# Optimization experiments

Measured on AMD Instinct MI355X. Metric: run time of the kernel, lower is better.

Reference implementation:

```python
import jax, jax.numpy as jnp
import numpy as np

B, N, DIM = 8, 2048, 512
HEADS, DIM_HEAD = 8, 64
INNER = HEADS * DIM_HEAD  # 512
SCALE = DIM_HEAD ** -0.5
NEG = -1e9


def setup_inputs() -> dict:
    key = jax.random.key(0)
    ks = jax.random.split(key, 7)
    x = jax.random.normal(ks[0], (B, N, DIM), dtype=jnp.float32)
    adj = jax.random.uniform(ks[1], (B, N, N), dtype=jnp.float32)
    att_mask = jax.random.randint(ks[2], (B, 1, N, N), 0, 2).astype(jnp.bool_)
    W_gcn = jax.random.normal(ks[3], (DIM, DIM), dtype=jnp.float32) * (DIM ** -0.5)
    W_qkv = jax.random.normal(ks[4], (DIM, 3 * INNER), dtype=jnp.float32) * (DIM ** -0.5)
    W_out = jax.random.normal(ks[5], (INNER + DIM, DIM), dtype=jnp.float32) * ((INNER + DIM) ** -0.5)
    b_out = jax.random.normal(ks[6], (DIM,), dtype=jnp.float32) * 0.01
    return {"x": x, "adj": adj, "att_mask": att_mask,
            "W_gcn": W_gcn, "W_qkv": W_qkv, "W_out": W_out, "b_out": b_out}


def reference(x, adj, att_mask, W_gcn, W_qkv, W_out, b_out):
    # GCN branch: adj @ (x W_gcn)  -> [b, n, dim]
    gcn = jnp.einsum('bnj,bjd->bnd', adj, x @ W_gcn)

    # Attention branch
    qkv = x @ W_qkv                                  # [b, n, 3*inner]
    q, k, v = jnp.split(qkv, 3, axis=-1)
    split_heads = lambda t: t.reshape(B, N, HEADS, DIM_HEAD).transpose(0, 2, 1, 3)
    q, k, v = split_heads(q), split_heads(k), split_heads(v)  # [b, h, n, d]

    dots = jnp.einsum('bhid,bhjd->bhij', q, k) * SCALE        # [b, h, n, n]
    dots = jnp.where(att_mask, NEG, dots)
    attn = jax.nn.softmax(dots, axis=-1)
    att_out = jnp.einsum('bhij,bhjd->bhid', attn, v)          # [b, h, n, d]
    att_out = att_out.transpose(0, 2, 1, 3).reshape(B, N, INNER)

    out = jnp.concatenate([att_out, gcn], axis=-1)            # [b, n, inner+dim]
    return out @ W_out + b_out                                # [b, n, dim]
```

## Files before the change

kernel.cpp:

```cpp
#include <hip/hip_runtime.h>
#include <stdint.h>

#define DEVFN __device__ __forceinline__

typedef __attribute__((ext_vector_type(8))) short short8;
typedef __attribute__((ext_vector_type(4))) short short4v;
typedef __attribute__((ext_vector_type(4))) float floatx4;
typedef __attribute__((ext_vector_type(16))) float floatx16;
typedef __attribute__((ext_vector_type(4))) float vfloat4;
typedef __attribute__((ext_vector_type(2))) unsigned int uint2v;
typedef __attribute__((ext_vector_type(4))) unsigned int uint4v;

#define MFMA_BF16(a,b,c) __builtin_amdgcn_mfma_f32_16x16x32_bf16((a),(b),(c),0,0,0)
#define MFMA32_BF16(a,b,c) __builtin_amdgcn_mfma_f32_32x32x16_bf16((a),(b),(c),0,0,0)
#define GL2LDS(g,l) __builtin_amdgcn_global_load_lds((const __attribute__((address_space(1))) void*)(g), (__attribute__((address_space(3))) void*)(l), 16, 0, 0)

DEVFN unsigned short f2bf(float f){
  unsigned u = __float_as_uint(f);
  u = (u + 0x7fffu + ((u >> 16) & 1u)) >> 16;
  return (unsigned short)u;
}

DEVFN unsigned cvtpk_bf16(float lo, float hi){
  unsigned r;
  asm("v_cvt_pk_bf16_f32 %0, %1, %2" : "=v"(r) : "v"(lo), "v"(hi));
  return r;
}

__global__ void detect_kernel(const unsigned char* m, unsigned int* flag){
  if (threadIdx.x == 0) *flag = 0u;
  __syncthreads();
  int any = 0;
  for (int i = threadIdx.x; i < 4096; i += 256)
    if ((i & 3) != 0 && m[i]) any = 1;
  if (any) atomicOr(flag, 1u);
}

__global__ void prep_kernel(const float* __restrict__ x, const float* __restrict__ wg,
                            const float* __restrict__ wq, const float* __restrict__ wo,
                            const void* __restrict__ mask, const unsigned* __restrict__ flag,
                            const float* __restrict__ adj,
                            unsigned short* __restrict__ xbf, unsigned short* __restrict__ wcat,
                            unsigned short* __restrict__ woutT, unsigned* __restrict__ mp,
                            unsigned short* __restrict__ adjb)
{
  int bid = blockIdx.x, tid = threadIdx.x;
  if (bid < 8192) {
    int i = (bid*256 + tid)*4;
    vfloat4 v = *(const vfloat4*)&x[i];
    short4v c; c[0]=(short)f2bf(v[0]); c[1]=(short)f2bf(v[1]); c[2]=(short)f2bf(v[2]); c[3]=(short)f2bf(v[3]);
    *(short4v*)&xbf[i] = c;
  } else if (bid < 8192 + 4096) {
    int i = (bid - 8192)*256 + tid;
    int k = i & 511, c = i >> 9;
    float v = (c < 512) ? wg[k*512 + c] : wq[k*1536 + (c - 512)];
    if (c >= 512 && c < 1024) v *= 0.18033688f;
    wcat[c*512 + k] = (unsigned short)f2bf(v);
  } else if (bid < 8192 + 4096 + 2048) {
    int i = (bid - 12288)*256 + tid;
    int k = i & 1023, n2 = i >> 10;
    woutT[n2*1024 + k] = (unsigned short)f2bf(wo[k*512 + n2]);
  } else if (bid < 145408) {
    int j = bid - 14336;
    int e = j*256 + tid;
    int v;
    if (*flag) v = ((const unsigned char*)mask)[e];
    else       v = ((const int*)mask)[e];
    unsigned long long ball = __ballot(v != 0);
    int base = e & ~63;
    int lane = tid & 63;
    if (lane == 0)  mp[(base >> 5) + 0] = (unsigned)(ball & 0xffffffffull);
    if (lane == 32) mp[(base >> 5) + 1] = (unsigned)(ball >> 32);
  } else {
    int i = ((bid - 145408)*256 + tid)*4;
    vfloat4 v = *(const vfloat4*)&adj[i];
    short4v c; c[0]=(short)f2bf(v[0]); c[1]=(short)f2bf(v[1]); c[2]=(short)f2bf(v[2]); c[3]=(short)f2bf(v[3]);
    *(short4v*)&adjb[i] = c;
  }
}

DEVFN void gemm_kloop_bf16(const unsigned short* Ag, int lda,
                           const unsigned short* Bg, int ldb, int K,
                           short* As, short* Bs, int w, int l,
                           floatx4 (&acc)[4][4])
{
  const int wr = (w >> 1)*64, wc = (w & 1)*64;
  for (int k0 = 0; k0 < K; k0 += 32) {
    __syncthreads();
#pragma unroll
    for (int i = 0; i < 2; i++) {
      int id = (w*2 + i)*64 + l;
      int row = id >> 2, part = id & 3;
      GL2LDS(Ag + row*lda + k0 + part*8, As + (w*2 + i)*512);
      GL2LDS(Bg + row*ldb + k0 + part*8, Bs + (w*2 + i)*512);
    }
    __syncthreads();
    short8 af[4], bfr[4];
#pragma unroll
    for (int t = 0; t < 4; t++) {
      af[t]  = *(const short8*)&As[(wr + t*16 + (l & 15))*32 + ((l >> 4) << 3)];
      bfr[t] = *(const short8*)&Bs[(wc + t*16 + (l & 15))*32 + ((l >> 4) << 3)];
    }
#pragma unroll
    for (int a2 = 0; a2 < 4; a2++)
#pragma unroll
      for (int b2 = 0; b2 < 4; b2++)
        acc[a2][b2] = MFMA_BF16(af[a2], bfr[b2], acc[a2][b2]);
  }
}

__global__ __launch_bounds__(256, 2)
void gemm_ab_kernel(const unsigned short* __restrict__ xbf, const unsigned short* __restrict__ wcat,
                    unsigned short* __restrict__ xgT, unsigned short* __restrict__ Qo,
                    unsigned short* __restrict__ Ko, unsigned short* __restrict__ VTo)
{
  __shared__ short lds[16384];
  int tid = threadIdx.x, w = tid >> 6, l = tid & 63;
  int bid = blockIdx.x;
  int xcd = bid & 7, slot = bid >> 3;
  int p  = xcd + ((slot >> 4) << 3);
  int nt = slot & 15;
  int rows0 = p*128, cols0 = nt*128;

  floatx4 acc[4][4];
  const floatx4 zf = {0.f, 0.f, 0.f, 0.f};
#pragma unroll
  for (int a2 = 0; a2 < 4; a2++)
#pragma unroll
    for (int b2 = 0; b2 < 4; b2++) acc[a2][b2] = zf;

  gemm_kloop_bf16(xbf + rows0*512, 512, wcat + cols0*512, 512, 512,
                  lds, lds + 4096, w, l, acc);
  __syncthreads();

  int wr = (w >> 1)*64, wc = (w & 1)*64;
  int b = p >> 4;
  int n0 = (p & 15)*128 + wr;
  int gc0 = cols0 + wc;

  if (nt < 4 || nt >= 12) {
    short* T = lds + w*4096;
#pragma unroll
    for (int mi = 0; mi < 4; mi++)
#pragma unroll
      for (int bi = 0; bi < 4; bi++)
#pragma unroll
        for (int r = 0; r < 4; r++) {
          int rl = mi*16 + ((l >> 4) << 2) + r;
          int cl = bi*16 + (l & 15);
          T[cl*64 + ((((rl >> 3) ^ (cl & 7))) << 3) + (rl & 7)] = (short)f2bf(acc[mi][bi][r]);
        }
#pragma unroll
    for (int i = 0; i < 8; i++) {
      int chunk = i*64 + l;
      int c = chunk >> 3, s = chunk & 7;
      short8 v = *(const short8*)&T[c*64 + ((s ^ (c & 7)) << 3)];
      int rowstart = n0 + s*8;
      if (nt < 4) {
        int d = gc0 + c;
        *(short8*)&xgT[(b*512 + d)*2048 + rowstart] = v;
      } else {
        int vc = gc0 + c - 1536;
        int hh = vc >> 6, dd = vc & 63;
        *(short8*)&VTo[((b*8 + hh)*64 + dd)*2048 + rowstart] = v;
      }
    }
  } else {
    unsigned short* dst = (nt < 8) ? Qo : Ko;
    int cbase = gc0 - ((nt < 8) ? 512 : 1024);
    int hh = cbase >> 6;
#pragma unroll
    for (int mi = 0; mi < 4; mi++)
#pragma unroll
      for (int bi = 0; bi < 4; bi++)
#pragma unroll
        for (int r = 0; r < 4; r++) {
          int rowg = n0 + mi*16 + ((l >> 4) << 2) + r;
          int dd = bi*16 + (l & 15);
          dst[((b*8 + hh)*2048 + rowg)*64 + dd] = (unsigned short)f2bf(acc[mi][bi][r]);
        }
  }
}

__global__ __launch_bounds__(256, 2)
void gemm_c_f32_kernel(const float* __restrict__ adj, const unsigned short* __restrict__ xgT,
                       unsigned short* __restrict__ cat)
{
  __shared__ short lds[8192];
  int tid = threadIdx.x, w = tid >> 6, l = tid & 63;
  int bid = blockIdx.x;
  int xcd = bid & 7, slot = bid >> 3;
  int p  = xcd + ((slot >> 2) << 3);
  int nt = slot & 3;
  int b = p >> 4, mt = p & 15;
  int rows0 = mt*128, cols0 = nt*128;
  const float* Ag = adj + (size_t)b*2048*2048 + (size_t)rows0*2048;
  const unsigned short* Bg = xgT + (b*512 + cols0)*2048;

  floatx4 acc[4][4];
  const floatx4 zf = {0.f, 0.f, 0.f, 0.f};
#pragma unroll
  for (int a2 = 0; a2 < 4; a2++)
#pragma unroll
    for (int b2 = 0; b2 < 4; b2++) acc[a2][b2] = zf;

  const int wr = (w >> 1)*64, wc = (w & 1)*64;
  for (int k0 = 0; k0 < 2048; k0 += 32) {
    __syncthreads();
#pragma unroll
    for (int i = 0; i < 4; i++) {
      int id = (w*4 + i)*64 + l;
      int row = id >> 3, part = id & 7;
      vfloat4 v = *(const vfloat4*)&Ag[row*2048 + k0 + part*4];
      short4v c4; c4[0]=(short)f2bf(v[0]); c4[1]=(short)f2bf(v[1]); c4[2]=(short)f2bf(v[2]); c4[3]=(short)f2bf(v[3]);
      *(short4v*)&lds[row*32 + part*4] = c4;
    }
#pragma unroll
    for (int i = 0; i < 2; i++) {
      int id = (w*2 + i)*64 + l;
      int row = id >> 2, part = id & 3;
      GL2LDS(Bg + row*2048 + k0 + part*8, lds + 4096 + (w*2 + i)*512);
    }
    __syncthreads();
    short8 af[4], bfr[4];
#pragma unroll
    for (int t = 0; t < 4; t++) {
      af[t]  = *(const short8*)&lds[(wr + t*16 + (l & 15))*32 + ((l >> 4) << 3)];
      bfr[t] = *(const short8*)&lds[4096 + (wc + t*16 + (l & 15))*32 + ((l >> 4) << 3)];
    }
#pragma unroll
    for (int a2 = 0; a2 < 4; a2++)
#pragma unroll
      for (int b2 = 0; b2 < 4; b2++)
        acc[a2][b2] = MFMA_BF16(af[a2], bfr[b2], acc[a2][b2]);
  }

#pragma unroll
  for (int mi = 0; mi < 4; mi++)
#pragma unroll
    for (int bi = 0; bi < 4; bi++)
#pragma unroll
      for (int r = 0; r < 4; r++) {
        int rowg = b*2048 + rows0 + wr + mi*16 + ((l >> 4) << 2) + r;
        int col  = 512 + cols0 + wc + bi*16 + (l & 15);
        cat[rowg*1024 + col] = (unsigned short)f2bf(acc[mi][bi][r]);
      }
}

DEVFN void attn_stage(const unsigned short* KB, const unsigned short* VB,
                      short* Ks, short* Vs, int kn0, int w, int l)
{
#pragma unroll
  for (int i = 0; i < 2; i++) {
    int id = (w*2 + i)*64 + l;
    int row = id >> 3, sl = id & 7;
    int sp = sl ^ (row & 7) ^ (((row >> 3) & 3) << 1);
    GL2LDS(KB + (kn0 + row)*64 + sp*8, Ks + (w*2 + i)*512);
    GL2LDS(VB + row*2048 + kn0 + sp*8, Vs + (w*2 + i)*512);
  }
}

DEVFN void attn_body(int abid, short* lds,
                     const unsigned short* __restrict__ Q, const unsigned short* __restrict__ Kb,
                     const unsigned short* __restrict__ VT, const unsigned* __restrict__ mp,
                     unsigned short* __restrict__ cat)
{
  int tid = threadIdx.x, w = tid >> 6, l = tid & 63;
  int c5 = l & 31, h = l >> 5;
  int hv = h*4;

  int xcd = abid & 7, slot = abid >> 3;
  int bh = xcd + ((slot >> 4) << 3);
  int qt = slot & 15;
  int b = bh >> 3, hd = bh & 7;
  int qw = qt*128 + w*32;

  const unsigned short* Qb = Q  + (size_t)bh*2048*64;
  const unsigned short* KB = Kb + (size_t)bh*2048*64;
  const unsigned short* VB = VT + (size_t)bh*64*2048;
  const unsigned* mrow = mp + b*2048*64 + (qw + c5)*64;

  short8 qf[4];
#pragma unroll
  for (int dk = 0; dk < 4; dk++)
    qf[dk] = *(const short8*)&Qb[(qw + c5)*64 + dk*16 + h*8];

  floatx16 oacc0, oacc1, nacc;
  const floatx16 zf16 = {0.f,0.f,0.f,0.f,0.f,0.f,0.f,0.f,0.f,0.f,0.f,0.f,0.f,0.f,0.f,0.f};
  oacc0 = zf16; oacc1 = zf16; nacc = zf16;

  const short8 ones8 = {(short)0x3F80,(short)0x3F80,(short)0x3F80,(short)0x3F80,
                        (short)0x3F80,(short)0x3F80,(short)0x3F80,(short)0x3F80};

  attn_stage(KB, VB, lds, lds + 8192, 0, w, l);
  uint2v wd = *(const uint2v*)&mrow[0];
  asm volatile("s_waitcnt vmcnt(0)" ::: "memory");
  __builtin_amdgcn_s_barrier();
  asm volatile("" ::: "memory");

  for (int kt = 0; kt < 32; kt++) {
    int cur = kt & 1;
    short* Ks = lds + cur*4096;
    short* Vs = lds + 8192 + cur*4096;

    if (kt < 31)
      attn_stage(KB, VB, lds + (cur ^ 1)*4096, lds + 8192 + (cur ^ 1)*4096, kt*64 + 64, w, l);

    uint2v wdn = wd;
    if (kt < 31) wdn = *(const uint2v*)&mrow[(kt + 1)*2];

#pragma unroll
    for (int kb = 0; kb < 2; kb++) {
      floatx16 sacc = zf16;
      __builtin_amdgcn_s_setprio(1);
#pragma unroll
      for (int dk = 0; dk < 4; dk++) {
        int row = kb*32 + c5;
        int sl = dk*2 + h;
        int sw = sl ^ (row & 7) ^ (((row >> 3) & 3) << 1);
        short8 kf = *(const short8*)&Ks[row*64 + (sw << 3)];
        sacc = MFMA32_BF16(kf, qf[dk], sacc);
      }
      __builtin_amdgcn_s_setprio(0);

      unsigned keep = ~((kb ? wd.y : wd.x) >> hv);
      float ps[16];
#pragma unroll
      for (int t = 0; t < 16; t++) {
        int pos = (t >> 2)*8 + (t & 3);
        int keepm = __builtin_amdgcn_sbfe((int)keep, pos, 1);
        float p = exp2f(sacc[t]);
        ps[t] = __uint_as_float(__float_as_uint(p) & (unsigned)keepm);
      }
      unsigned pk[4][2];
#pragma unroll
      for (int s = 0; s < 4; s++) {
        pk[s][0] = cvtpk_bf16(ps[s*4 + 0], ps[s*4 + 1]);
        pk[s][1] = cvtpk_bf16(ps[s*4 + 2], ps[s*4 + 3]);
      }

#pragma unroll
      for (int ksl = 0; ksl < 2; ksl++) {
        uint2v s0 = __builtin_amdgcn_permlane32_swap(pk[2*ksl][0], pk[2*ksl + 1][0], false, false);
        uint2v s1 = __builtin_amdgcn_permlane32_swap(pk[2*ksl][1], pk[2*ksl + 1][1], false, false);
        uint4v fu;
        fu[0] = s0.x;
        fu[1] = s1.x;
        fu[2] = s0.y;
        fu[3] = s1.y;
        short8 pfrag = *(short8*)&fu;

        __builtin_amdgcn_s_setprio(1);
#pragma unroll
        for (int db = 0; db < 2; db++) {
          int row = db*32 + c5;
          int sl = kb*4 + ksl*2 + h;
          int sw = sl ^ (row & 7) ^ (((row >> 3) & 3) << 1);
          short8 vf = *(const short8*)&Vs[row*64 + (sw << 3)];
          if (db == 0) oacc0 = MFMA32_BF16(pfrag, vf, oacc0);
          else         oacc1 = MFMA32_BF16(pfrag, vf, oacc1);
        }
        nacc = MFMA32_BF16(pfrag, ones8, nacc);
        __builtin_amdgcn_s_setprio(0);
      }
    }
    wd = wdn;

    asm volatile("s_waitcnt vmcnt(0)" ::: "memory");
    __builtin_amdgcn_s_barrier();
    asm volatile("" ::: "memory");
  }

#pragma unroll
  for (int t = 0; t < 16; t++) {
    float iv = 1.0f / nacc[t];
    int qrow = qw + (t & 3) + 8*(t >> 2) + hv;
    unsigned short* orow = &cat[(b*2048 + qrow)*1024 + hd*64];
    orow[c5]      = (unsigned short)f2bf(oacc0[t] * iv);
    orow[32 + c5] = (unsigned short)f2bf(oacc1[t] * iv);
  }
}

__global__ __launch_bounds__(256, 4)
void attn_kernel(const unsigned short* __restrict__ Q, const unsigned short* __restrict__ Kb,
                 const unsigned short* __restrict__ VT, const unsigned* __restrict__ mp,
                 unsigned short* __restrict__ cat)
{
  __shared__ short lds[16384];
  attn_body(blockIdx.x, lds, Q, Kb, VT, mp, cat);
}

__global__ __launch_bounds__(256, 3)
void fused_ca_kernel(const unsigned short* __restrict__ adjb, const unsigned short* __restrict__ xgT,
                     const unsigned short* __restrict__ Q, const unsigned short* __restrict__ Kb,
                     const unsigned short* __restrict__ VT, const unsigned* __restrict__ mp,
                     unsigned short* __restrict__ cat)
{
  __shared__ short lds[16384];
  int bid = blockIdx.x;
  int r3 = bid % 3;
  if (r3 == 2) {
    int cbid = bid / 3;
    int tid = threadIdx.x, w = tid >> 6, l = tid & 63;
    int xcd = cbid & 7, slot = cbid >> 3;
    int p  = xcd + ((slot >> 2) << 3);
    int nt = slot & 3;
    int b = p >> 4, mt = p & 15;
    int rows0 = mt*128, cols0 = nt*128;

    floatx4 acc[4][4];
    const floatx4 zf = {0.f, 0.f, 0.f, 0.f};
#pragma unroll
    for (int a2 = 0; a2 < 4; a2++)
#pragma unroll
      for (int b2 = 0; b2 < 4; b2++) acc[a2][b2] = zf;

    gemm_kloop_bf16(adjb + (size_t)b*2048*2048 + (size_t)rows0*2048, 2048,
                    xgT + (b*512 + cols0)*2048, 2048, 2048,
                    lds, lds + 4096, w, l, acc);

    int wr = (w >> 1)*64, wc = (w & 1)*64;
#pragma unroll
    for (int mi = 0; mi < 4; mi++)
#pragma unroll
      for (int bi = 0; bi < 4; bi++)
#pragma unroll
        for (int r = 0; r < 4; r++) {
          int rowg = b*2048 + rows0 + wr + mi*16 + ((l >> 4) << 2) + r;
          int col  = 512 + cols0 + wc + bi*16 + (l & 15);
          cat[rowg*1024 + col] = (unsigned short)f2bf(acc[mi][bi][r]);
        }
  } else {
    int abid = (bid / 3)*2 + r3;
    attn_body(abid, lds, Q, Kb, VT, mp, cat);
  }
}

__global__ __launch_bounds__(256, 2)
void gemm_d_kernel(const unsigned short* __restrict__ cat, const unsigned short* __restrict__ woutT,
                   const float* __restrict__ bout, float* __restrict__ out)
{
  __shared__ short lds[8192];
  int tid = threadIdx.x, w = tid >> 6, l = tid & 63;
  int bid = blockIdx.x;
  int xcd = bid & 7, slot = bid >> 3;
  int p  = xcd + ((slot >> 2) << 3);
  int nt = slot & 3;
  int rows0 = p*128, cols0 = nt*128;

  floatx4 acc[4][4];
  const floatx4 zf = {0.f, 0.f, 0.f, 0.f};
#pragma unroll
  for (int a2 = 0; a2 < 4; a2++)
#pragma unroll
    for (int b2 = 0; b2 < 4; b2++) acc[a2][b2] = zf;

  gemm_kloop_bf16(cat + (size_t)rows0*1024, 1024, woutT + cols0*1024, 1024, 1024,
                  lds, lds + 4096, w, l, acc);

  int wr = (w >> 1)*64, wc = (w & 1)*64;
#pragma unroll
  for (int bi = 0; bi < 4; bi++) {
    int col = cols0 + wc + bi*16 + (l & 15);
    float bias = bout[col];
#pragma unroll
    for (int mi = 0; mi < 4; mi++)
#pragma unroll
      for (int r = 0; r < 4; r++) {
        int rowg = rows0 + wr + mi*16 + ((l >> 4) << 2) + r;
        out[rowg*512 + col] = acc[mi][bi][r] + bias;
      }
  }
}

extern "C" void kernel_launch(void* const* d_in, const int* in_sizes, int n_in,
                              void* d_out, int out_size, void* d_ws, size_t ws_size,
                              hipStream_t stream)
{
  (void)in_sizes; (void)n_in; (void)out_size;
  const float* x   = (const float*)d_in[0];
  const float* adj = (const float*)d_in[1];
  const void*  msk = d_in[2];
  const float* wg  = (const float*)d_in[3];
  const float* wq  = (const float*)d_in[4];
  const float* wo  = (const float*)d_in[5];
  const float* bo  = (const float*)d_in[6];
  float* out = (float*)d_out;
  char* ws = (char*)d_ws;

  unsigned short* xbf   = (unsigned short*)(ws + 0);
  unsigned short* wcat  = (unsigned short*)(ws + 16777216);
  unsigned short* woutT = (unsigned short*)(ws + 18874368);
  unsigned short* xgT   = (unsigned short*)(ws + 19922944);
  unsigned short* Qb    = (unsigned short*)(ws + 36700160);
  unsigned short* Kb    = (unsigned short*)(ws + 53477376);
  unsigned short* VTb   = (unsigned short*)(ws + 70254592);
  unsigned short* cat   = (unsigned short*)(ws + 87031808);
  unsigned*       mp    = (unsigned*)(ws + 120586240);
  unsigned*       flag  = (unsigned*)(ws + 124780544);
  unsigned short* adjb  = (unsigned short*)(ws + 124780608);

  const int use_adjb = (ws_size >= (size_t)124780608 + 67108864) ? 1 : 0;

  detect_kernel<<<1, 256, 0, stream>>>((const unsigned char*)msk, flag);
  prep_kernel<<<use_adjb ? 178176 : 145408, 256, 0, stream>>>(
      x, wg, wq, wo, msk, flag, adj, xbf, wcat, woutT, mp, adjb);
  gemm_ab_kernel<<<2048, 256, 0, stream>>>(xbf, wcat, xgT, Qb, Kb, VTb);
  if (use_adjb) {
    fused_ca_kernel<<<1536, 256, 0, stream>>>(adjb, xgT, Qb, Kb, VTb, mp, cat);
  } else {
    gemm_c_f32_kernel<<<512, 256, 0, stream>>>(adj, xgT, cat);
    attn_kernel<<<1024, 256, 0, stream>>>(Qb, Kb, VTb, mp, cat);
  }
  gemm_d_kernel<<<512, 256, 0, stream>>>(cat, woutT, bo, out);
}
```

Before: 377.7 us.

## Overlap mask packing and adj bf16 conversion with QKV GEMM blocks

Moves the mask bit-packing and the adj fp32-to-bf16 conversion out of the prep kernel and into extra blocks of the QKV/GCN projection GEMM launch. Blocks are interleaved 2 GEMM : 7 memory blocks, so bandwidth-bound conversion work runs alongside compute-bound MFMA work. The conversion blocks are also made coarser, each looping over many elements. In exchange, the GEMM kernel carries more register/LDS pressure from the extra code path, and the block-to-tile mapping changes, which could affect XCD locality.

```diff
diff --git a/kernel.cpp b/kernel.cpp
--- a/kernel.cpp
+++ b/kernel.cpp
@@ -36,13 +36,10 @@
   if (any) atomicOr(flag, 1u);
 }
 
-__global__ void prep_kernel(const float* __restrict__ x, const float* __restrict__ wg,
-                            const float* __restrict__ wq, const float* __restrict__ wo,
-                            const void* __restrict__ mask, const unsigned* __restrict__ flag,
-                            const float* __restrict__ adj,
-                            unsigned short* __restrict__ xbf, unsigned short* __restrict__ wcat,
-                            unsigned short* __restrict__ woutT, unsigned* __restrict__ mp,
-                            unsigned short* __restrict__ adjb)
+__global__ void prep_small_kernel(const float* __restrict__ x, const float* __restrict__ wg,
+                                  const float* __restrict__ wq, const float* __restrict__ wo,
+                                  unsigned short* __restrict__ xbf, unsigned short* __restrict__ wcat,
+                                  unsigned short* __restrict__ woutT)
 {
   int bid = blockIdx.x, tid = threadIdx.x;
   if (bid < 8192) {
@@ -50,17 +47,42 @@
     vfloat4 v = *(const vfloat4*)&x[i];
     short4v c; c[0]=(short)f2bf(v[0]); c[1]=(short)f2bf(v[1]); c[2]=(short)f2bf(v[2]); c[3]=(short)f2bf(v[3]);
     *(short4v*)&xbf[i] = c;
-  } else if (bid < 8192 + 4096) {
+  } else if (bid < 12288) {
     int i = (bid - 8192)*256 + tid;
     int k = i & 511, c = i >> 9;
     float v = (c < 512) ? wg[k*512 + c] : wq[k*1536 + (c - 512)];
     if (c >= 512 && c < 1024) v *= 0.18033688f;
     wcat[c*512 + k] = (unsigned short)f2bf(v);
-  } else if (bid < 8192 + 4096 + 2048) {
+  } else {
     int i = (bid - 12288)*256 + tid;
     int k = i & 1023, n2 = i >> 10;
     woutT[n2*1024 + k] = (unsigned short)f2bf(wo[k*512 + n2]);
-  } else if (bid < 145408) {
+  }
+}
+
+__global__ void prep_full_kernel(const float* __restrict__ x, const float* __restrict__ wg,
+                                 const float* __restrict__ wq, const float* __restrict__ wo,
+                                 const void* __restrict__ mask, const unsigned* __restrict__ flag,
+                                 unsigned short* __restrict__ xbf, unsigned short* __restrict__ wcat,
+                                 unsigned short* __restrict__ woutT, unsigned* __restrict__ mp)
+{
+  int bid = blockIdx.x, tid = threadIdx.x;
+  if (bid < 8192) {
+    int i = (bid*256 + tid)*4;
+    vfloat4 v = *(const vfloat4*)&x[i];
+    short4v c; c[0]=(short)f2bf(v[0]); c[1]=(short)f2bf(v[1]); c[2]=(short)f2bf(v[2]); c[3]=(short)f2bf(v[3]);
+    *(short4v*)&xbf[i] = c;
+  } else if (bid < 12288) {
+    int i = (bid - 8192)*256 + tid;
+    int k = i & 511, c = i >> 9;
+    float v = (c < 512) ? wg[k*512 + c] : wq[k*1536 + (c - 512)];
+    if (c >= 512 && c < 1024) v *= 0.18033688f;
+    wcat[c*512 + k] = (unsigned short)f2bf(v);
+  } else if (bid < 14336) {
+    int i = (bid - 12288)*256 + tid;
+    int k = i & 1023, n2 = i >> 10;
+    woutT[n2*1024 + k] = (unsigned short)f2bf(wo[k*512 + n2]);
+  } else {
     int j = bid - 14336;
     int e = j*256 + tid;
     int v;
@@ -71,11 +93,6 @@
     int lane = tid & 63;
     if (lane == 0)  mp[(base >> 5) + 0] = (unsigned)(ball & 0xffffffffull);
     if (lane == 32) mp[(base >> 5) + 1] = (unsigned)(ball >> 32);
-  } else {
-    int i = ((bid - 145408)*256 + tid)*4;
-    vfloat4 v = *(const vfloat4*)&adj[i];
-    short4v c; c[0]=(short)f2bf(v[0]); c[1]=(short)f2bf(v[1]); c[2]=(short)f2bf(v[2]); c[3]=(short)f2bf(v[3]);
-    *(short4v*)&adjb[i] = c;
   }
 }
 
@@ -112,12 +129,51 @@
 __global__ __launch_bounds__(256, 2)
 void gemm_ab_kernel(const unsigned short* __restrict__ xbf, const unsigned short* __restrict__ wcat,
                     unsigned short* __restrict__ xgT, unsigned short* __restrict__ Qo,
-                    unsigned short* __restrict__ Ko, unsigned short* __restrict__ VTo)
+                    unsigned short* __restrict__ Ko, unsigned short* __restrict__ VTo,
+                    const void* __restrict__ mask, const unsigned* __restrict__ flag,
+                    const float* __restrict__ adj,
+                    unsigned* __restrict__ mp, unsigned short* __restrict__ adjb,
+                    int mode)
 {
   __shared__ short lds[16384];
   int tid = threadIdx.x, w = tid >> 6, l = tid & 63;
   int bid = blockIdx.x;
-  int xcd = bid & 7, slot = bid >> 3;
+
+  int gemmid;
+  if (mode) {
+    int r9 = bid % 9, g9 = bid / 9;
+    if (r9 >= 2) {
+      int bw = g9*7 + (r9 - 2);
+      if (bw < 2048) {
+        unsigned fl = *flag;
+        int lane = tid & 63;
+        for (int it = 0; it < 64; it++) {
+          int e = (bw*64 + it)*256 + tid;
+          int v;
+          if (fl) v = ((const unsigned char*)mask)[e];
+          else    v = ((const int*)mask)[e];
+          unsigned long long ball = __ballot(v != 0);
+          int base = e & ~63;
+          if (lane == 0)  mp[(base >> 5) + 0] = (unsigned)(ball & 0xffffffffull);
+          if (lane == 32) mp[(base >> 5) + 1] = (unsigned)(ball >> 32);
+        }
+      } else if (bw < 6144) {
+        int ab = bw - 2048;
+        for (int it = 0; it < 8; it++) {
+          int i = ((ab*8 + it)*256 + tid)*4;
+          vfloat4 v = *(const vfloat4*)&adj[i];
+          short4v c; c[0]=(short)f2bf(v[0]); c[1]=(short)f2bf(v[1]); c[2]=(short)f2bf(v[2]); c[3]=(short)f2bf(v[3]);
+          *(short4v*)&adjb[i] = c;
+        }
+      }
+      return;
+    }
+    gemmid = g9*2 + r9;
+  } else {
+    gemmid = bid;
+  }
+
+  int xcd = gemmid & 7, slot = gemmid >> 3;
   int p  = xcd + ((slot >> 4) << 3);
   int nt = slot & 15;
   int rows0 = p*128, cols0 = nt*128;
@@ -503,12 +559,16 @@
   const int use_adjb = (ws_size >= (size_t)124780608 + 67108864) ? 1 : 0;
 
   detect_kernel<<<1, 256, 0, stream>>>((const unsigned char*)msk, flag);
-  prep_kernel<<<use_adjb ? 178176 : 145408, 256, 0, stream>>>(
-      x, wg, wq, wo, msk, flag, adj, xbf, wcat, woutT, mp, adjb);
-  gemm_ab_kernel<<<2048, 256, 0, stream>>>(xbf, wcat, xgT, Qb, Kb, VTb);
   if (use_adjb) {
+    prep_small_kernel<<<14336, 256, 0, stream>>>(x, wg, wq, wo, xbf, wcat, woutT);
+    gemm_ab_kernel<<<9216, 256, 0, stream>>>(xbf, wcat, xgT, Qb, Kb, VTb,
+                                             msk, flag, adj, mp, adjb, 1);
     fused_ca_kernel<<<1536, 256, 0, stream>>>(adjb, xgT, Qb, Kb, VTb, mp, cat);
   } else {
+    prep_full_kernel<<<145408, 256, 0, stream>>>(x, wg, wq, wo, msk, flag,
+                                                 xbf, wcat, woutT, mp);
+    gemm_ab_kernel<<<2048, 256, 0, stream>>>(xbf, wcat, xgT, Qb, Kb, VTb,
+                                             msk, flag, adj, mp, adjb, 0);
     gemm_c_f32_kernel<<<512, 256, 0, stream>>>(adj, xgT, cat);
     attn_kernel<<<1024, 256, 0, stream>>>(Qb, Kb, VTb, mp, cat);
   }
```

Result: slower. 450.1 us (+19.2%).
